# Optimization experiments

Measured on AMD Instinct MI355X. Metric: run time of the kernel, lower is better.

The kernel has to match this reference:

```python
import jax, jax.numpy as jnp
import numpy as np

B, S, D = 4, 4096, 1280
SKV, CD = 77, 2048
H = 20
HD = D // H  # 64
IP_SCALE = 1.0  # self.scale * call-time scale


def setup_inputs() -> dict:
    key = jax.random.key(0)
    ks = jax.random.split(key, 10)
    w = lambda k, sh: jax.random.normal(k, sh, jnp.float32) * 0.02
    return {
        "hidden_states": jax.random.normal(ks[0], (B, S, D), jnp.float32),
        "encoder_hidden_states": jax.random.normal(ks[1], (B, SKV, CD), jnp.float32),
        "scca_mask": jax.random.uniform(ks[2], (1, 1, 64, 64), jnp.float32),
        "Wq": w(ks[3], (D, D)),
        "Wk": w(ks[4], (CD, D)),
        "Wv": w(ks[5], (CD, D)),
        "Wk_ip": w(ks[6], (CD, D)),
        "Wv_ip": w(ks[7], (CD, D)),
        "Wo": w(ks[8], (D, D)),
        "bo": jnp.zeros((D,), jnp.float32),
    }


def _split_heads(x):
    b, n, _ = x.shape
    return x.reshape(b, n, H, HD).transpose(0, 2, 1, 3)  # [B,H,N,HD]


def _attention(q, k, v):
    # naive softmax(QK^T / sqrt(d)) V, matching attn.get_attention_scores + bmm
    qh, kh, vh = _split_heads(q), _split_heads(k), _split_heads(v)
    scores = jnp.einsum("bhqd,bhkd->bhqk", qh, kh) * (1.0 / np.sqrt(HD)).astype(np.float32)
    probs = jax.nn.softmax(scores, axis=-1)
    out = jnp.einsum("bhqk,bhkd->bhqd", probs, vh)
    b = q.shape[0]
    return out.transpose(0, 2, 1, 3).reshape(b, -1, D)


def reference(hidden_states, encoder_hidden_states, scca_mask, Wq, Wk, Wv, Wk_ip, Wv_ip, Wo, bo):
    # base cross-attention branch
    q = hidden_states @ Wq
    k = encoder_hidden_states @ Wk
    v = encoder_hidden_states @ Wv
    hs = _attention(q, k, v)

    # IP-adapter branch (same queries, separate k/v projections)
    k_ip = encoder_hidden_states @ Wk_ip
    v_ip = encoder_hidden_states @ Wv_ip
    hs_ip = _attention(q, k_ip, v_ip)

    # SCCA mask: bilinear downsample to (h,h), h = sqrt(seq_len)
    h = int(S ** 0.5)
    mask_down = jax.image.resize(scca_mask, (1, 1, h, h), method="bilinear")  # align_corners=False
    mask_flat = mask_down.reshape(1, -1, 1)  # [1, S, 1]
    hs_ip = hs_ip * mask_flat
    ratio = mask_flat.mean()
    boost = jnp.where(
        (ratio > 1e-6) & (ratio < 0.1),
        jnp.minimum(1.0 + (0.1 - ratio) * 30.0, 4.0),
        jnp.float32(1.0),
    )
    hs_ip = hs_ip * boost

    hs = hs + IP_SCALE * hs_ip
    # to_out[0] linear + to_out[1] dropout (identity at eval)
    out = hs @ Wo + bo
    return out
```

## Files before the change

### kernel.cpp

```cpp
#include <hip/hip_runtime.h>
#include <hip/hip_bf16.h>
#include <stdint.h>

#define B_   4
#define S_   4096
#define D_   1280
#define H_   20
#define HD_  64
#define SKV_ 77
#define CD_  2048

typedef short bfrag8 __attribute__((ext_vector_type(8)));
typedef float f32x4  __attribute__((ext_vector_type(4)));

__device__ __forceinline__ float bf2f(unsigned short h) {
  return __uint_as_float(((unsigned int)h) << 16);
}
__device__ __forceinline__ unsigned short f2bf(float f) {
  unsigned int u = __float_as_uint(f);
  unsigned int r = (u + 0x7FFFu + ((u >> 16) & 1u)) >> 16;
  return (unsigned short)r;
}
__device__ __forceinline__ float cvtlo(unsigned int u) { return __uint_as_float(u << 16); }
__device__ __forceinline__ float cvthi(unsigned int u) { return __uint_as_float(u & 0xFFFF0000u); }

__device__ __forceinline__ void async16(const unsigned short* g, unsigned short* l) {
  __builtin_amdgcn_global_load_lds(
      (const __attribute__((address_space(1))) unsigned int*)g,
      (__attribute__((address_space(3))) unsigned int*)l, 16, 0, 0);
}

struct PrepArgs {
  const float* csrc[6]; unsigned short* cdst[6]; int cn4[6];
  const float* tsrc[2]; unsigned short* tdst[2];
  const float* mask; float* boostp;
};

__global__ __launch_bounds__(256) void prep_k(PrepArgs a) {
  const int y = blockIdx.y;
  if (y < 6) {
    const float* __restrict__ src = a.csrc[y];
    unsigned short* __restrict__ dst = a.cdst[y];
    const int n4 = a.cn4[y];
    for (int i = blockIdx.x * 256 + threadIdx.x; i < n4; i += gridDim.x * 256) {
      float4 v = ((const float4*)src)[i];
      uint2 o;
      o.x = (unsigned int)f2bf(v.x) | ((unsigned int)f2bf(v.y) << 16);
      o.y = (unsigned int)f2bf(v.z) | ((unsigned int)f2bf(v.w) << 16);
      ((uint2*)dst)[i] = o;
    }
  } else if (y < 8) {
    if (blockIdx.x >= 40 * 40) return;
    const float* __restrict__ src = a.tsrc[y - 6];
    unsigned short* __restrict__ dst = a.tdst[y - 6];
    __shared__ float t[32][33];
    const int k0 = (blockIdx.x / 40) * 32, n0 = (blockIdx.x % 40) * 32;
    const int r = threadIdx.x >> 3, c4 = threadIdx.x & 7;
    float4 v = *(const float4*)(src + (size_t)(k0 + r) * D_ + n0 + c4 * 4);
    t[r][c4 * 4 + 0] = v.x; t[r][c4 * 4 + 1] = v.y;
    t[r][c4 * 4 + 2] = v.z; t[r][c4 * 4 + 3] = v.w;
    __syncthreads();
    uint2 o;
    o.x = (unsigned int)f2bf(t[c4 * 4 + 0][r]) | ((unsigned int)f2bf(t[c4 * 4 + 1][r]) << 16);
    o.y = (unsigned int)f2bf(t[c4 * 4 + 2][r]) | ((unsigned int)f2bf(t[c4 * 4 + 3][r]) << 16);
    *(uint2*)(dst + (size_t)(n0 + r) * D_ + k0 + c4 * 4) = o;
  } else {
    if (blockIdx.x != 0) return;
    __shared__ float red[4];
    float s = 0.f;
    for (int i = threadIdx.x; i < S_; i += 256) s += a.mask[i];
#pragma unroll
    for (int off = 32; off > 0; off >>= 1) s += __shfl_down(s, off, 64);
    int wave = threadIdx.x >> 6, lane = threadIdx.x & 63;
    if (lane == 0) red[wave] = s;
    __syncthreads();
    if (threadIdx.x == 0) {
      float t = red[0] + red[1] + red[2] + red[3];
      float ratio = t * (1.0f / (float)S_);
      float boost = (ratio > 1e-6f && ratio < 0.1f)
                        ? fminf(1.0f + (0.1f - ratio) * 30.0f, 4.0f)
                        : 1.0f;
      a.boostp[0] = boost;
    }
  }
}

__global__ __launch_bounds__(512, 2) void gemm4b(
    const unsigned short* __restrict__ A, const unsigned short* __restrict__ Bt,
    void* __restrict__ C, int M, int N, int K,
    const float* __restrict__ bias, int f32out) {
  __shared__ unsigned short Asm[4 * 256 * 32];
  __shared__ unsigned short Bsm[4 * 128 * 32];

  const int tid = threadIdx.x;
  const int nb = N >> 7;
  int wg = blockIdx.x;
  {
    int cpx = gridDim.x >> 3;
    wg = (wg & 7) * cpx + (wg >> 3);
  }
  const int m0 = (wg / nb) * 256, n0 = (wg % nb) * 128;

  const int wave = tid >> 6, lane = tid & 63;
  const int wm = (wave >> 1) * 64, wn = (wave & 1) * 64;
  const int l16 = lane & 15, quad = lane >> 4;

  const int r0 = tid >> 2;
  const int gch = ((tid & 3) - (tid >> 3)) & 3;
  const int ch = (quad + (l16 >> 1)) & 3;

  const unsigned short* srcA = A + (size_t)(m0 + r0) * K + gch * 8;
  const unsigned short* srcB = Bt + (size_t)(n0 + r0) * K + gch * 8;

  const int NH = K >> 5;

  auto stageA = [&](unsigned short* dst, int h) {
    const unsigned short* s = srcA + h * 32;
    async16(s, dst + tid * 8);
    async16(s + (size_t)128 * K, dst + (512 + tid) * 8);
  };
  auto stageB = [&](unsigned short* dst, int h) {
    async16(srcB + h * 32, dst + tid * 8);
  };

  f32x4 acc[4][4] = {};

  stageA(Asm + 0 * 8192, 0); stageB(Bsm + 0 * 4096, 0);
  stageA(Asm + 1 * 8192, 1); stageB(Bsm + 1 * 4096, 1);
  stageA(Asm + 2 * 8192, 2); stageB(Bsm + 2 * 4096, 2);
  asm volatile("s_waitcnt vmcnt(6)" ::: "memory");
  __builtin_amdgcn_s_barrier();

  for (int h = 0; h < NH; ++h) {
    unsigned short* cura = Asm + (h & 3) * 8192;
    unsigned short* curb = Bsm + (h & 3) * 4096;
    const int hp = h + 3;
    const bool pre = hp < NH;
    unsigned short* pa = Asm + (hp & 3) * 8192;
    unsigned short* pb = Bsm + (hp & 3) * 4096;

    bfrag8 af0 = *(const bfrag8*)(cura + (wm + 0 * 16 + l16) * 32 + ch * 8);
    bfrag8 af1 = *(const bfrag8*)(cura + (wm + 1 * 16 + l16) * 32 + ch * 8);
    bfrag8 bf[4];
#pragma unroll
    for (int nt = 0; nt < 4; ++nt)
      bf[nt] = *(const bfrag8*)(curb + (wn + nt * 16 + l16) * 32 + ch * 8);
    if (pre) stageA(pa, hp);
    __builtin_amdgcn_s_barrier();
    __builtin_amdgcn_s_setprio(1);
#pragma unroll
    for (int nt = 0; nt < 4; ++nt) {
      acc[0][nt] = __builtin_amdgcn_mfma_f32_16x16x32_bf16(af0, bf[nt], acc[0][nt], 0, 0, 0);
      acc[1][nt] = __builtin_amdgcn_mfma_f32_16x16x32_bf16(af1, bf[nt], acc[1][nt], 0, 0, 0);
    }
    __builtin_amdgcn_s_setprio(0);
    __builtin_amdgcn_s_barrier();
    bfrag8 af2 = *(const bfrag8*)(cura + (wm + 2 * 16 + l16) * 32 + ch * 8);
    bfrag8 af3 = *(const bfrag8*)(cura + (wm + 3 * 16 + l16) * 32 + ch * 8);
    if (pre) stageB(pb, hp);
    __builtin_amdgcn_s_barrier();
    __builtin_amdgcn_s_setprio(1);
#pragma unroll
    for (int nt = 0; nt < 4; ++nt) {
      acc[2][nt] = __builtin_amdgcn_mfma_f32_16x16x32_bf16(af2, bf[nt], acc[2][nt], 0, 0, 0);
      acc[3][nt] = __builtin_amdgcn_mfma_f32_16x16x32_bf16(af3, bf[nt], acc[3][nt], 0, 0, 0);
    }
    __builtin_amdgcn_s_setprio(0);
    if (h + 1 < NH) {
      int inflight = NH - 2 - h;
      if (inflight >= 2)      { asm volatile("s_waitcnt vmcnt(6)" ::: "memory"); }
      else if (inflight == 1) { asm volatile("s_waitcnt vmcnt(3)" ::: "memory"); }
      else                    { asm volatile("s_waitcnt vmcnt(0)" ::: "memory"); }
      __builtin_amdgcn_s_barrier();
    }
  }

#pragma unroll
  for (int mt = 0; mt < 4; ++mt) {
#pragma unroll
    for (int nt = 0; nt < 4; ++nt) {
#pragma unroll
      for (int r = 0; r < 4; ++r) {
        int row = m0 + wm + mt * 16 + quad * 4 + r;
        int col = n0 + wn + nt * 16 + l16;
        float v = acc[mt][nt][r];
        if (bias) v += bias[col];
        if (f32out) ((float*)C)[(size_t)row * N + col] = v;
        else ((unsigned short*)C)[(size_t)row * N + col] = f2bf(v);
      }
    }
  }
}

struct KVArgs { const unsigned short* W[4]; unsigned short* O[4]; };
__global__ __launch_bounds__(256) void gemm_kv4(
    const unsigned short* __restrict__ A, KVArgs kv, int M, int N, int K) {
  const unsigned short* __restrict__ Bw = kv.W[blockIdx.z];
  unsigned short* __restrict__ C = kv.O[blockIdx.z];
  __shared__ unsigned short As[64][40];
  __shared__ unsigned short Bs[64][40];

  const int tid = threadIdx.x;
  const int m0 = blockIdx.x * 64, n0 = blockIdx.y * 64;
  const int wave = tid >> 6, lane = tid & 63;
  const int l16 = lane & 15, quad = lane >> 4;

  f32x4 acc[4] = {};

  for (int k0 = 0; k0 < K; k0 += 32) {
    {
      int row = tid >> 2, kc = tid & 3;
      int gr = m0 + row;
      uint4 v = make_uint4(0u, 0u, 0u, 0u);
      if (gr < M) v = *(const uint4*)(A + (size_t)gr * K + k0 + kc * 8);
      *(uint4*)&As[row][kc * 8] = v;
    }
    {
      int kk = tid >> 3, n8 = tid & 7;
      uint4 v = *(const uint4*)(Bw + (size_t)(k0 + kk) * N + n0 + n8 * 8);
      unsigned short* p = (unsigned short*)&v;
#pragma unroll
      for (int j = 0; j < 8; ++j) Bs[n8 * 8 + j][kk] = p[j];
    }
    __syncthreads();

    bfrag8 af = *(const bfrag8*)&As[wave * 16 + l16][quad * 8];
#pragma unroll
    for (int nt = 0; nt < 4; ++nt) {
      bfrag8 bf = *(const bfrag8*)&Bs[nt * 16 + l16][quad * 8];
      acc[nt] = __builtin_amdgcn_mfma_f32_16x16x32_bf16(af, bf, acc[nt], 0, 0, 0);
    }
    __syncthreads();
  }

#pragma unroll
  for (int nt = 0; nt < 4; ++nt) {
#pragma unroll
    for (int r = 0; r < 4; ++r) {
      int row = m0 + wave * 16 + quad * 4 + r;
      if (row < M) {
        int col = n0 + nt * 16 + l16;
        C[(size_t)row * N + col] = f2bf(acc[nt][r]);
      }
    }
  }
}

__global__ __launch_bounds__(256, 2) void attn_k(
    const unsigned short* __restrict__ Q, const unsigned short* __restrict__ Kb,
    const unsigned short* __restrict__ Vb, const unsigned short* __restrict__ Kip,
    const unsigned short* __restrict__ Vip, const float* __restrict__ mask,
    const float* __restrict__ boostp, unsigned short* __restrict__ hs) {
  __shared__ unsigned short Ks0[80 * 88];
  __shared__ unsigned short Ks1[80 * 88];
  __shared__ unsigned short VT0[64 * 104];
  __shared__ unsigned short VT1[64 * 104];
  __shared__ unsigned short Ps[4 * 16 * 104];

  const int tid = threadIdx.x;
  const int bh = blockIdx.y;
  const int b = bh / H_, h = bh % H_;
  const int qb = blockIdx.x * 64;
  const int wave = tid >> 6, lane = tid & 63;
  const int l16 = lane & 15, quad = lane >> 4;

  bfrag8 qf[2];
  {
    const unsigned short* qp =
        Q + (size_t)(b * S_ + qb + wave * 16 + l16) * D_ + h * HD_ + quad * 8;
    qf[0] = *(const bfrag8*)(qp);
    qf[1] = *(const bfrag8*)(qp + 32);
  }

  auto stageK = [&](const unsigned short* src, unsigned short* dst) {
    for (int idx = tid; idx < 640; idx += 256) {
      int row = idx >> 3, c = idx & 7;
      uint4 v = make_uint4(0u, 0u, 0u, 0u);
      if (row < SKV_)
        v = *(const uint4*)(src + (size_t)(b * SKV_ + row) * D_ + h * HD_ + c * 8);
      *(uint4*)(dst + row * 88 + c * 8) = v;
    }
  };
  auto stageVT = [&](const unsigned short* src, unsigned short* dst) {
    for (int idx = tid; idx < 384; idx += 256) {
      int kp = idx % 48, c = idx / 48;
      int k0 = kp * 2;
      uint4 a = make_uint4(0u, 0u, 0u, 0u), bb = make_uint4(0u, 0u, 0u, 0u);
      if (k0 < SKV_)
        a = *(const uint4*)(src + (size_t)(b * SKV_ + k0) * D_ + h * HD_ + c * 8);
      if (k0 + 1 < SKV_)
        bb = *(const uint4*)(src + (size_t)(b * SKV_ + k0 + 1) * D_ + h * HD_ + c * 8);
      const unsigned short* ap = (const unsigned short*)&a;
      const unsigned short* bp = (const unsigned short*)&bb;
#pragma unroll
      for (int j = 0; j < 8; ++j) {
        int d = c * 8 + j;
        *(unsigned int*)(dst + d * 104 + k0) =
            (unsigned int)ap[j] | ((unsigned int)bp[j] << 16);
      }
    }
  };

  stageK(Kb, Ks0);
  stageK(Kip, Ks1);
  stageVT(Vb, VT0);
  stageVT(Vip, VT1);

  {
    unsigned short* pw = Ps + wave * 16 * 104;
    int rr = lane >> 2, w4 = lane & 3;
    *(unsigned int*)(pw + rr * 104 + 80 + w4 * 4) = 0u;
    *(unsigned int*)(pw + rr * 104 + 82 + w4 * 4) = 0u;
  }
  __syncthreads();

  struct PVOut { f32x4 a[4]; float inv; };

  auto branch = [&](const unsigned short* KsL, const unsigned short* VTL) -> PVOut {
    f32x4 st[5] = {};
#pragma unroll
    for (int t = 0; t < 5; ++t) {
      const unsigned short* kb = KsL + (t * 16 + l16) * 88 + quad * 8;
      bfrag8 k0 = *(const bfrag8*)(kb);
      bfrag8 k1 = *(const bfrag8*)(kb + 32);
      st[t] = __builtin_amdgcn_mfma_f32_16x16x32_bf16(k0, qf[0], st[t], 0, 0, 0);
      st[t] = __builtin_amdgcn_mfma_f32_16x16x32_bf16(k1, qf[1], st[t], 0, 0, 0);
    }
    float p[5][4];
    float m = -1e30f;
#pragma unroll
    for (int t = 0; t < 5; ++t)
#pragma unroll
      for (int r = 0; r < 4; ++r) {
        float s = st[t][r] * 0.125f;
        if (t == 4 && r >= 1) s = (quad == 3) ? -1e30f : s;
        p[t][r] = s;
        m = fmaxf(m, s);
      }
    m = fmaxf(m, __shfl_xor(m, 16, 64));
    m = fmaxf(m, __shfl_xor(m, 32, 64));
    float l = 0.f;
#pragma unroll
    for (int t = 0; t < 5; ++t)
#pragma unroll
      for (int r = 0; r < 4; ++r) {
        float e = __expf(p[t][r] - m);
        p[t][r] = e;
        l += e;
      }
    l += __shfl_xor(l, 16, 64);
    l += __shfl_xor(l, 32, 64);

    unsigned short* prow = Ps + wave * 16 * 104 + l16 * 104 + quad * 4;
#pragma unroll
    for (int t = 0; t < 5; ++t) {
      __hip_bfloat162 h0 = __float22bfloat162_rn(make_float2(p[t][0], p[t][1]));
      __hip_bfloat162 h1 = __float22bfloat162_rn(make_float2(p[t][2], p[t][3]));
      unsigned int u0, u1;
      __builtin_memcpy(&u0, &h0, 4);
      __builtin_memcpy(&u1, &h1, 4);
      *(unsigned int*)(prow + t * 16) = u0;
      *(unsigned int*)(prow + t * 16 + 2) = u1;
    }
    __syncthreads();

    PVOut o;
    f32x4 acc[4] = {};
    const unsigned short* pbase = Ps + wave * 16 * 104 + l16 * 104;
#pragma unroll
    for (int ks = 0; ks < 3; ++ks) {
      bfrag8 pf = *(const bfrag8*)(pbase + ks * 32 + quad * 8);
#pragma unroll
      for (int dt = 0; dt < 4; ++dt) {
        bfrag8 vf = *(const bfrag8*)(VTL + (dt * 16 + l16) * 104 + ks * 32 + quad * 8);
        acc[dt] = __builtin_amdgcn_mfma_f32_16x16x32_bf16(pf, vf, acc[dt], 0, 0, 0);
      }
    }
#pragma unroll
    for (int dt = 0; dt < 4; ++dt) o.a[dt] = acc[dt];
    o.inv = 1.0f / l;
    return o;
  };

  PVOut o0 = branch(Ks0, VT0);
  __syncthreads();
  PVOut o1 = branch(Ks1, VT1);

  const float boost = boostp[0];
#pragma unroll
  for (int r = 0; r < 4; ++r) {
    const int s = qb + wave * 16 + quad * 4 + r;
    const float sc = mask[s] * boost;
    const float i0 = __shfl(o0.inv, quad * 4 + r, 64);
    const float i1 = __shfl(o1.inv, quad * 4 + r, 64);
    unsigned short* op = hs + (size_t)(b * S_ + s) * D_ + h * HD_ + l16;
#pragma unroll
    for (int dt = 0; dt < 4; ++dt) {
      float v = o0.a[dt][r] * i0 + sc * (o1.a[dt][r] * i1);
      op[dt * 16] = f2bf(v);
    }
  }
}

extern "C" void kernel_launch(void* const* d_in, const int* in_sizes, int n_in,
                              void* d_out, int out_size, void* d_ws, size_t ws_size,
                              hipStream_t stream) {
  const float* hidden = (const float*)d_in[0];
  const float* enc    = (const float*)d_in[1];
  const float* mask   = (const float*)d_in[2];
  const float* Wq     = (const float*)d_in[3];
  const float* Wk     = (const float*)d_in[4];
  const float* Wv     = (const float*)d_in[5];
  const float* Wkip   = (const float*)d_in[6];
  const float* Wvip   = (const float*)d_in[7];
  const float* Wo     = (const float*)d_in[8];
  const float* bo     = (const float*)d_in[9];

  char* ws = (char*)d_ws;
  unsigned short* cHid  = (unsigned short*)(ws + 0ULL);
  unsigned short* hsb   = cHid;
  unsigned short* cEnc  = (unsigned short*)(ws + 41943040ULL);
  unsigned short* cWqT  = (unsigned short*)(ws + 43204608ULL);
  unsigned short* cWk   = (unsigned short*)(ws + 46481408ULL);
  unsigned short* cWv   = (unsigned short*)(ws + 51724288ULL);
  unsigned short* cWkip = (unsigned short*)(ws + 56967168ULL);
  unsigned short* cWvip = (unsigned short*)(ws + 62210048ULL);
  unsigned short* cWoT  = (unsigned short*)(ws + 67452928ULL);
  unsigned short* Qb    = (unsigned short*)(ws + 70729728ULL);
  unsigned short* Kb    = (unsigned short*)(ws + 112672768ULL);
  unsigned short* Vb    = (unsigned short*)(ws + 113461248ULL);
  unsigned short* Kip   = (unsigned short*)(ws + 114249728ULL);
  unsigned short* Vip   = (unsigned short*)(ws + 115038208ULL);
  float* boostp         = (float*)(ws + 115826688ULL);

  {
    PrepArgs a;
    a.csrc[0] = hidden; a.cdst[0] = cHid;  a.cn4[0] = (B_ * S_ * D_) >> 2;
    a.csrc[1] = enc;    a.cdst[1] = cEnc;  a.cn4[1] = (B_ * SKV_ * CD_) >> 2;
    a.csrc[2] = Wk;     a.cdst[2] = cWk;   a.cn4[2] = (CD_ * D_) >> 2;
    a.csrc[3] = Wv;     a.cdst[3] = cWv;   a.cn4[3] = (CD_ * D_) >> 2;
    a.csrc[4] = Wkip;   a.cdst[4] = cWkip; a.cn4[4] = (CD_ * D_) >> 2;
    a.csrc[5] = Wvip;   a.cdst[5] = cWvip; a.cn4[5] = (CD_ * D_) >> 2;
    a.tsrc[0] = Wq; a.tdst[0] = cWqT;
    a.tsrc[1] = Wo; a.tdst[1] = cWoT;
    a.mask = mask; a.boostp = boostp;
    prep_k<<<dim3(2048, 9), dim3(256), 0, stream>>>(a);
  }

  const int MQ = B_ * S_;
  const int MKV = B_ * SKV_;

  gemm4b<<<dim3((MQ / 256) * (D_ / 128)), dim3(512), 0, stream>>>(
      cHid, cWqT, Qb, MQ, D_, D_, nullptr, 0);

  {
    KVArgs kv;
    kv.W[0] = cWk;   kv.O[0] = Kb;
    kv.W[1] = cWv;   kv.O[1] = Vb;
    kv.W[2] = cWkip; kv.O[2] = Kip;
    kv.W[3] = cWvip; kv.O[3] = Vip;
    gemm_kv4<<<dim3(5, 20, 4), dim3(256), 0, stream>>>(cEnc, kv, MKV, D_, CD_);
  }

  attn_k<<<dim3(S_ / 64, B_ * H_), dim3(256), 0, stream>>>(Qb, Kb, Vb, Kip, Vip,
                                                           mask, boostp, hsb);

  gemm4b<<<dim3((MQ / 256) * (D_ / 128)), dim3(512), 0, stream>>>(
      hsb, cWoT, d_out, MQ, D_, D_, bo, 1);
}
```

Baseline: 548.7 us.

## Use triple-buffered GEMM pipelines and a wide 128x256 tile for Q projection

The Q projection GEMM moves to a new kernel with 256 threads and a 128x256 output tile per block (128-column slice per wave), triple-buffered in shared memory. The output projection uses a triple-buffered version of the old 256x128 kernel with rotating buffer pointers and a launch bound of 3 blocks per CU instead of 2. The aim is to cut LDS use so more blocks fit per CU and to raise MFMA work per fragment load in the Q GEMM. The cost is a shallower prefetch depth, and the wide kernel's 128 accumulator registers per thread may limit occupancy.

```diff
diff --git a/kernel.cpp b/kernel.cpp
--- a/kernel.cpp
+++ b/kernel.cpp
@@ -85,12 +85,12 @@
   }
 }
 
-__global__ __launch_bounds__(512, 2) void gemm4b(
+__global__ __launch_bounds__(512, 3) void gemm8p(
     const unsigned short* __restrict__ A, const unsigned short* __restrict__ Bt,
     void* __restrict__ C, int M, int N, int K,
     const float* __restrict__ bias, int f32out) {
-  __shared__ unsigned short Asm[4 * 256 * 32];
-  __shared__ unsigned short Bsm[4 * 128 * 32];
+  __shared__ unsigned short Asm[3 * 256 * 32];
+  __shared__ unsigned short Bsm[3 * 128 * 32];
 
   const int tid = threadIdx.x;
   const int nb = N >> 7;
@@ -112,40 +112,40 @@
   const unsigned short* srcA = A + (size_t)(m0 + r0) * K + gch * 8;
   const unsigned short* srcB = Bt + (size_t)(n0 + r0) * K + gch * 8;
 
-  const int NH = K >> 5;
-
-  auto stageA = [&](unsigned short* dst, int h) {
-    const unsigned short* s = srcA + h * 32;
+  unsigned short* pa0 = Asm;
+  unsigned short* pa1 = Asm + 256 * 32;
+  unsigned short* pa2 = Asm + 2 * 256 * 32;
+  unsigned short* pb0 = Bsm;
+  unsigned short* pb1 = Bsm + 128 * 32;
+  unsigned short* pb2 = Bsm + 2 * 128 * 32;
+
+  const int NT = K >> 5;
+
+  auto stageA = [&](unsigned short* dst, int t) {
+    const unsigned short* s = srcA + t * 32;
     async16(s, dst + tid * 8);
     async16(s + (size_t)128 * K, dst + (512 + tid) * 8);
   };
-  auto stageB = [&](unsigned short* dst, int h) {
-    async16(srcB + h * 32, dst + tid * 8);
+  auto stageB = [&](unsigned short* dst, int t) {
+    async16(srcB + t * 32, dst + tid * 8);
   };
 
   f32x4 acc[4][4] = {};
 
-  stageA(Asm + 0 * 8192, 0); stageB(Bsm + 0 * 4096, 0);
-  stageA(Asm + 1 * 8192, 1); stageB(Bsm + 1 * 4096, 1);
-  stageA(Asm + 2 * 8192, 2); stageB(Bsm + 2 * 4096, 2);
-  asm volatile("s_waitcnt vmcnt(6)" ::: "memory");
+  stageA(pa0, 0); stageB(pb0, 0);
+  stageA(pa1, 1); stageB(pb1, 1);
+  asm volatile("s_waitcnt vmcnt(3)" ::: "memory");
   __builtin_amdgcn_s_barrier();
 
-  for (int h = 0; h < NH; ++h) {
-    unsigned short* cura = Asm + (h & 3) * 8192;
-    unsigned short* curb = Bsm + (h & 3) * 4096;
-    const int hp = h + 3;
-    const bool pre = hp < NH;
-    unsigned short* pa = Asm + (hp & 3) * 8192;
-    unsigned short* pb = Bsm + (hp & 3) * 4096;
-
-    bfrag8 af0 = *(const bfrag8*)(cura + (wm + 0 * 16 + l16) * 32 + ch * 8);
-    bfrag8 af1 = *(const bfrag8*)(cura + (wm + 1 * 16 + l16) * 32 + ch * 8);
+  for (int t = 0; t < NT; ++t) {
+    const bool pre = (t + 2) < NT;
+    bfrag8 af0 = *(const bfrag8*)(pa0 + (wm + 0 * 16 + l16) * 32 + ch * 8);
+    bfrag8 af1 = *(const bfrag8*)(pa0 + (wm + 1 * 16 + l16) * 32 + ch * 8);
     bfrag8 bf[4];
 #pragma unroll
     for (int nt = 0; nt < 4; ++nt)
-      bf[nt] = *(const bfrag8*)(curb + (wn + nt * 16 + l16) * 32 + ch * 8);
-    if (pre) stageA(pa, hp);
+      bf[nt] = *(const bfrag8*)(pb0 + (wn + nt * 16 + l16) * 32 + ch * 8);
+    if (pre) stageA(pa2, t + 2);
     __builtin_amdgcn_s_barrier();
     __builtin_amdgcn_s_setprio(1);
 #pragma unroll
@@ -155,9 +155,9 @@
     }
     __builtin_amdgcn_s_setprio(0);
     __builtin_amdgcn_s_barrier();
-    bfrag8 af2 = *(const bfrag8*)(cura + (wm + 2 * 16 + l16) * 32 + ch * 8);
-    bfrag8 af3 = *(const bfrag8*)(cura + (wm + 3 * 16 + l16) * 32 + ch * 8);
-    if (pre) stageB(pb, hp);
+    bfrag8 af2 = *(const bfrag8*)(pa0 + (wm + 2 * 16 + l16) * 32 + ch * 8);
+    bfrag8 af3 = *(const bfrag8*)(pa0 + (wm + 3 * 16 + l16) * 32 + ch * 8);
+    if (pre) stageB(pb2, t + 2);
     __builtin_amdgcn_s_barrier();
     __builtin_amdgcn_s_setprio(1);
 #pragma unroll
@@ -166,12 +166,12 @@
       acc[3][nt] = __builtin_amdgcn_mfma_f32_16x16x32_bf16(af3, bf[nt], acc[3][nt], 0, 0, 0);
     }
     __builtin_amdgcn_s_setprio(0);
-    if (h + 1 < NH) {
-      int inflight = NH - 2 - h;
-      if (inflight >= 2)      { asm volatile("s_waitcnt vmcnt(6)" ::: "memory"); }
-      else if (inflight == 1) { asm volatile("s_waitcnt vmcnt(3)" ::: "memory"); }
-      else                    { asm volatile("s_waitcnt vmcnt(0)" ::: "memory"); }
+    if (t + 1 < NT) {
+      if (pre) { asm volatile("s_waitcnt vmcnt(3)" ::: "memory"); }
+      else     { asm volatile("s_waitcnt vmcnt(0)" ::: "memory"); }
       __builtin_amdgcn_s_barrier();
+      unsigned short* ta = pa0; pa0 = pa1; pa1 = pa2; pa2 = ta;
+      unsigned short* tb = pb0; pb0 = pb1; pb1 = pb2; pb2 = tb;
     }
   }
 
@@ -179,6 +179,117 @@
   for (int mt = 0; mt < 4; ++mt) {
 #pragma unroll
     for (int nt = 0; nt < 4; ++nt) {
+#pragma unroll
+      for (int r = 0; r < 4; ++r) {
+        int row = m0 + wm + mt * 16 + quad * 4 + r;
+        int col = n0 + wn + nt * 16 + l16;
+        float v = acc[mt][nt][r];
+        if (bias) v += bias[col];
+        if (f32out) ((float*)C)[(size_t)row * N + col] = v;
+        else ((unsigned short*)C)[(size_t)row * N + col] = f2bf(v);
+      }
+    }
+  }
+}
+
+__global__ __launch_bounds__(256, 2) void gemm_wide(
+    const unsigned short* __restrict__ A, const unsigned short* __restrict__ Bt,
+    void* __restrict__ C, int M, int N, int K,
+    const float* __restrict__ bias, int f32out) {
+  __shared__ unsigned short Asm[3 * 128 * 32];
+  __shared__ unsigned short Bsm[3 * 256 * 32];
+
+  const int tid = threadIdx.x;
+  const int nb = N >> 8;
+  int wg = blockIdx.x;
+  {
+    int cpx = gridDim.x >> 3;
+    wg = (wg & 7) * cpx + (wg >> 3);
+  }
+  const int m0 = (wg / nb) * 128, n0 = (wg % nb) * 256;
+
+  const int wave = tid >> 6, lane = tid & 63;
+  const int wm = (wave >> 1) * 64, wn = (wave & 1) * 128;
+  const int l16 = lane & 15, quad = lane >> 4;
+
+  const int r0 = tid >> 2;
+  const int gch = ((tid & 3) - (tid >> 3)) & 3;
+  const int ch = (quad + (l16 >> 1)) & 3;
+
+  const unsigned short* srcA = A + (size_t)(m0 + r0) * K + gch * 8;
+  const unsigned short* srcB = Bt + (size_t)(n0 + r0) * K + gch * 8;
+
+  unsigned short* pa0 = Asm;
+  unsigned short* pa1 = Asm + 128 * 32;
+  unsigned short* pa2 = Asm + 2 * 128 * 32;
+  unsigned short* pb0 = Bsm;
+  unsigned short* pb1 = Bsm + 256 * 32;
+  unsigned short* pb2 = Bsm + 2 * 256 * 32;
+
+  const int NT = K >> 5;
+
+  auto stageA = [&](unsigned short* dst, int t) {
+    const unsigned short* s = srcA + t * 32;
+    async16(s, dst + tid * 8);
+    async16(s + (size_t)64 * K, dst + (256 + tid) * 8);
+  };
+  auto stageB = [&](unsigned short* dst, int t) {
+    const unsigned short* s = srcB + t * 32;
+    async16(s, dst + tid * 8);
+    async16(s + (size_t)64 * K, dst + (256 + tid) * 8);
+    async16(s + (size_t)128 * K, dst + (512 + tid) * 8);
+    async16(s + (size_t)192 * K, dst + (768 + tid) * 8);
+  };
+
+  f32x4 acc[4][8] = {};
+
+  stageA(pa0, 0); stageB(pb0, 0);
+  stageA(pa1, 1); stageB(pb1, 1);
+  asm volatile("s_waitcnt vmcnt(6)" ::: "memory");
+  __builtin_amdgcn_s_barrier();
+
+  for (int t = 0; t < NT; ++t) {
+    const bool pre = (t + 2) < NT;
+    bfrag8 af0 = *(const bfrag8*)(pa0 + (wm + 0 * 16 + l16) * 32 + ch * 8);
+    bfrag8 af1 = *(const bfrag8*)(pa0 + (wm + 1 * 16 + l16) * 32 + ch * 8);
+    bfrag8 bf[8];
+#pragma unroll
+    for (int nt = 0; nt < 8; ++nt)
+      bf[nt] = *(const bfrag8*)(pb0 + (wn + nt * 16 + l16) * 32 + ch * 8);
+    if (pre) stageA(pa2, t + 2);
+    __builtin_amdgcn_s_barrier();
+    __builtin_amdgcn_s_setprio(1);
+#pragma unroll
+    for (int nt = 0; nt < 8; ++nt) {
+      acc[0][nt] = __builtin_amdgcn_mfma_f32_16x16x32_bf16(af0, bf[nt], acc[0][nt], 0, 0, 0);
+      acc[1][nt] = __builtin_amdgcn_mfma_f32_16x16x32_bf16(af1, bf[nt], acc[1][nt], 0, 0, 0);
+    }
+    __builtin_amdgcn_s_setprio(0);
+    __builtin_amdgcn_s_barrier();
+    bfrag8 af2 = *(const bfrag8*)(pa0 + (wm + 2 * 16 + l16) * 32 + ch * 8);
+    bfrag8 af3 = *(const bfrag8*)(pa0 + (wm + 3 * 16 + l16) * 32 + ch * 8);
+    if (pre) stageB(pb2, t + 2);
+    __builtin_amdgcn_s_barrier();
+    __builtin_amdgcn_s_setprio(1);
+#pragma unroll
+    for (int nt = 0; nt < 8; ++nt) {
+      acc[2][nt] = __builtin_amdgcn_mfma_f32_16x16x32_bf16(af2, bf[nt], acc[2][nt], 0, 0, 0);
+      acc[3][nt] = __builtin_amdgcn_mfma_f32_16x16x32_bf16(af3, bf[nt], acc[3][nt], 0, 0, 0);
+    }
+    __builtin_amdgcn_s_setprio(0);
+    if (t + 1 < NT) {
+      if (pre) { asm volatile("s_waitcnt vmcnt(6)" ::: "memory"); }
+      else     { asm volatile("s_waitcnt vmcnt(0)" ::: "memory"); }
+      __builtin_amdgcn_s_barrier();
+      unsigned short* ta = pa0; pa0 = pa1; pa1 = pa2; pa2 = ta;
+      unsigned short* tb = pb0; pb0 = pb1; pb1 = pb2; pb2 = tb;
+    }
+  }
+
+#pragma unroll
+  for (int mt = 0; mt < 4; ++mt) {
+#pragma unroll
+    for (int nt = 0; nt < 8; ++nt) {
 #pragma unroll
       for (int r = 0; r < 4; ++r) {
         int row = m0 + wm + mt * 16 + quad * 4 + r;
@@ -450,7 +561,7 @@
   const int MQ = B_ * S_;
   const int MKV = B_ * SKV_;
 
-  gemm4b<<<dim3((MQ / 256) * (D_ / 128)), dim3(512), 0, stream>>>(
+  gemm_wide<<<dim3((MQ / 128) * (D_ / 256)), dim3(256), 0, stream>>>(
       cHid, cWqT, Qb, MQ, D_, D_, nullptr, 0);
 
   {
@@ -465,6 +576,6 @@
   attn_k<<<dim3(S_ / 64, B_ * H_), dim3(256), 0, stream>>>(Qb, Kb, Vb, Kip, Vip,
                                                            mask, boostp, hsb);
 
-  gemm4b<<<dim3((MQ / 256) * (D_ / 128)), dim3(512), 0, stream>>>(
+  gemm8p<<<dim3((MQ / 256) * (D_ / 128)), dim3(512), 0, stream>>>(
       hsb, cWoT, d_out, MQ, D_, D_, bo, 1);
 }
```

New measurement: 502.8 us. 8.4% less time.

## Replace GEMM with 128x256 tile, 4-wave kernel using triple-buffered LDS rotation

Applied to the files above, without the earlier changes.

The Q and output projection GEMM now uses 256 threads per block. Each block computes a 128x256 tile with a 64x128 subtile per wave instead of a 256x128 tile, and the shared memory pipeline drops from four buffers to three rotating pointer buffers with prefetch distance two. The aim is more MFMA work per fragment load and fewer blocks with less LDS each. In exchange it uses more accumulator registers (128 floats per thread), which risks register pressure or spills, and it has a shallower prefetch pipeline.

```diff
diff --git a/kernel.cpp b/kernel.cpp
--- a/kernel.cpp
+++ b/kernel.cpp
@@ -85,24 +85,24 @@
   }
 }
 
-__global__ __launch_bounds__(512, 2) void gemm4b(
+__global__ __launch_bounds__(256, 2) void gemm_wide(
     const unsigned short* __restrict__ A, const unsigned short* __restrict__ Bt,
     void* __restrict__ C, int M, int N, int K,
     const float* __restrict__ bias, int f32out) {
-  __shared__ unsigned short Asm[4 * 256 * 32];
-  __shared__ unsigned short Bsm[4 * 128 * 32];
+  __shared__ unsigned short Asm[3 * 128 * 32];
+  __shared__ unsigned short Bsm[3 * 256 * 32];
 
   const int tid = threadIdx.x;
-  const int nb = N >> 7;
+  const int nb = N >> 8;
   int wg = blockIdx.x;
   {
     int cpx = gridDim.x >> 3;
     wg = (wg & 7) * cpx + (wg >> 3);
   }
-  const int m0 = (wg / nb) * 256, n0 = (wg % nb) * 128;
+  const int m0 = (wg / nb) * 128, n0 = (wg % nb) * 256;
 
   const int wave = tid >> 6, lane = tid & 63;
-  const int wm = (wave >> 1) * 64, wn = (wave & 1) * 64;
+  const int wm = (wave >> 1) * 64, wn = (wave & 1) * 128;
   const int l16 = lane & 15, quad = lane >> 4;
 
   const int r0 = tid >> 2;
@@ -112,73 +112,77 @@
   const unsigned short* srcA = A + (size_t)(m0 + r0) * K + gch * 8;
   const unsigned short* srcB = Bt + (size_t)(n0 + r0) * K + gch * 8;
 
-  const int NH = K >> 5;
-
-  auto stageA = [&](unsigned short* dst, int h) {
-    const unsigned short* s = srcA + h * 32;
+  unsigned short* pa0 = Asm;
+  unsigned short* pa1 = Asm + 128 * 32;
+  unsigned short* pa2 = Asm + 2 * 128 * 32;
+  unsigned short* pb0 = Bsm;
+  unsigned short* pb1 = Bsm + 256 * 32;
+  unsigned short* pb2 = Bsm + 2 * 256 * 32;
+
+  const int NT = K >> 5;
+
+  auto stageA = [&](unsigned short* dst, int t) {
+    const unsigned short* s = srcA + t * 32;
     async16(s, dst + tid * 8);
+    async16(s + (size_t)64 * K, dst + (256 + tid) * 8);
+  };
+  auto stageB = [&](unsigned short* dst, int t) {
+    const unsigned short* s = srcB + t * 32;
+    async16(s, dst + tid * 8);
+    async16(s + (size_t)64 * K, dst + (256 + tid) * 8);
     async16(s + (size_t)128 * K, dst + (512 + tid) * 8);
+    async16(s + (size_t)192 * K, dst + (768 + tid) * 8);
   };
-  auto stageB = [&](unsigned short* dst, int h) {
-    async16(srcB + h * 32, dst + tid * 8);
-  };
-
-  f32x4 acc[4][4] = {};
-
-  stageA(Asm + 0 * 8192, 0); stageB(Bsm + 0 * 4096, 0);
-  stageA(Asm + 1 * 8192, 1); stageB(Bsm + 1 * 4096, 1);
-  stageA(Asm + 2 * 8192, 2); stageB(Bsm + 2 * 4096, 2);
+
+  f32x4 acc[4][8] = {};
+
+  stageA(pa0, 0); stageB(pb0, 0);
+  stageA(pa1, 1); stageB(pb1, 1);
   asm volatile("s_waitcnt vmcnt(6)" ::: "memory");
   __builtin_amdgcn_s_barrier();
 
-  for (int h = 0; h < NH; ++h) {
-    unsigned short* cura = Asm + (h & 3) * 8192;
-    unsigned short* curb = Bsm + (h & 3) * 4096;
-    const int hp = h + 3;
-    const bool pre = hp < NH;
-    unsigned short* pa = Asm + (hp & 3) * 8192;
-    unsigned short* pb = Bsm + (hp & 3) * 4096;
-
-    bfrag8 af0 = *(const bfrag8*)(cura + (wm + 0 * 16 + l16) * 32 + ch * 8);
-    bfrag8 af1 = *(const bfrag8*)(cura + (wm + 1 * 16 + l16) * 32 + ch * 8);
-    bfrag8 bf[4];
-#pragma unroll
-    for (int nt = 0; nt < 4; ++nt)
-      bf[nt] = *(const bfrag8*)(curb + (wn + nt * 16 + l16) * 32 + ch * 8);
-    if (pre) stageA(pa, hp);
+  for (int t = 0; t < NT; ++t) {
+    const bool pre = (t + 2) < NT;
+    bfrag8 af0 = *(const bfrag8*)(pa0 + (wm + 0 * 16 + l16) * 32 + ch * 8);
+    bfrag8 af1 = *(const bfrag8*)(pa0 + (wm + 1 * 16 + l16) * 32 + ch * 8);
+    bfrag8 bf[8];
+#pragma unroll
+    for (int nt = 0; nt < 8; ++nt)
+      bf[nt] = *(const bfrag8*)(pb0 + (wn + nt * 16 + l16) * 32 + ch * 8);
+    if (pre) stageA(pa2, t + 2);
     __builtin_amdgcn_s_barrier();
     __builtin_amdgcn_s_setprio(1);
 #pragma unroll
-    for (int nt = 0; nt < 4; ++nt) {
+    for (int nt = 0; nt < 8; ++nt) {
       acc[0][nt] = __builtin_amdgcn_mfma_f32_16x16x32_bf16(af0, bf[nt], acc[0][nt], 0, 0, 0);
       acc[1][nt] = __builtin_amdgcn_mfma_f32_16x16x32_bf16(af1, bf[nt], acc[1][nt], 0, 0, 0);
     }
     __builtin_amdgcn_s_setprio(0);
     __builtin_amdgcn_s_barrier();
-    bfrag8 af2 = *(const bfrag8*)(cura + (wm + 2 * 16 + l16) * 32 + ch * 8);
-    bfrag8 af3 = *(const bfrag8*)(cura + (wm + 3 * 16 + l16) * 32 + ch * 8);
-    if (pre) stageB(pb, hp);
+    bfrag8 af2 = *(const bfrag8*)(pa0 + (wm + 2 * 16 + l16) * 32 + ch * 8);
+    bfrag8 af3 = *(const bfrag8*)(pa0 + (wm + 3 * 16 + l16) * 32 + ch * 8);
+    if (pre) stageB(pb2, t + 2);
     __builtin_amdgcn_s_barrier();
     __builtin_amdgcn_s_setprio(1);
 #pragma unroll
-    for (int nt = 0; nt < 4; ++nt) {
+    for (int nt = 0; nt < 8; ++nt) {
       acc[2][nt] = __builtin_amdgcn_mfma_f32_16x16x32_bf16(af2, bf[nt], acc[2][nt], 0, 0, 0);
       acc[3][nt] = __builtin_amdgcn_mfma_f32_16x16x32_bf16(af3, bf[nt], acc[3][nt], 0, 0, 0);
     }
     __builtin_amdgcn_s_setprio(0);
-    if (h + 1 < NH) {
-      int inflight = NH - 2 - h;
-      if (inflight >= 2)      { asm volatile("s_waitcnt vmcnt(6)" ::: "memory"); }
-      else if (inflight == 1) { asm volatile("s_waitcnt vmcnt(3)" ::: "memory"); }
-      else                    { asm volatile("s_waitcnt vmcnt(0)" ::: "memory"); }
+    if (t + 1 < NT) {
+      if (pre) { asm volatile("s_waitcnt vmcnt(6)" ::: "memory"); }
+      else     { asm volatile("s_waitcnt vmcnt(0)" ::: "memory"); }
       __builtin_amdgcn_s_barrier();
+      unsigned short* ta = pa0; pa0 = pa1; pa1 = pa2; pa2 = ta;
+      unsigned short* tb = pb0; pb0 = pb1; pb1 = pb2; pb2 = tb;
     }
   }
 
 #pragma unroll
   for (int mt = 0; mt < 4; ++mt) {
 #pragma unroll
-    for (int nt = 0; nt < 4; ++nt) {
+    for (int nt = 0; nt < 8; ++nt) {
 #pragma unroll
       for (int r = 0; r < 4; ++r) {
         int row = m0 + wm + mt * 16 + quad * 4 + r;
@@ -450,7 +454,7 @@
   const int MQ = B_ * S_;
   const int MKV = B_ * SKV_;
 
-  gemm4b<<<dim3((MQ / 256) * (D_ / 128)), dim3(512), 0, stream>>>(
+  gemm_wide<<<dim3((MQ / 128) * (D_ / 256)), dim3(256), 0, stream>>>(
       cHid, cWqT, Qb, MQ, D_, D_, nullptr, 0);
 
   {
@@ -465,6 +469,6 @@
   attn_k<<<dim3(S_ / 64, B_ * H_), dim3(256), 0, stream>>>(Qb, Kb, Vb, Kip, Vip,
                                                            mask, boostp, hsb);
 
-  gemm4b<<<dim3((MQ / 256) * (D_ / 128)), dim3(512), 0, stream>>>(
+  gemm_wide<<<dim3((MQ / 128) * (D_ / 256)), dim3(256), 0, stream>>>(
       hsb, cWoT, d_out, MQ, D_, D_, bo, 1);
 }
```

Result: faster. 518.5 us (-5.5%).
